# Kernel tuning notes

Hardware: AMD Instinct MI355X
Metric: run time of the kernel (lower is better)

Reference implementation:

```python
import jax, jax.numpy as jnp
import numpy as np

TEMPERATURE = 1.0
CLAMP = 10.0

def setup_inputs() -> dict:
    key = jax.random.key(0)
    k1, k2, kw, kb, km = jax.random.split(key, 5)
    B, N1, N2, D = 8, 2048, 2048, 256
    features1 = jax.random.normal(k1, (B, N1, D), dtype=jnp.float32)
    features2 = jax.random.normal(k2, (B, N2, D), dtype=jnp.float32)
    # Linear(D, D) params (torch convention: y = x @ W.T + b)
    W = jax.random.normal(kw, (D, D), dtype=jnp.float32) * (1.0 / np.sqrt(D))
    b = jax.random.normal(kb, (D,), dtype=jnp.float32) * 0.02
    # learnable metric matrix (initialized near identity, small perturbation)
    metric = jnp.eye(D, dtype=jnp.float32) + 0.01 * jax.random.normal(km, (D, D), dtype=jnp.float32)
    return {"features1": features1, "features2": features2, "W": W, "b": b, "metric": metric}

def reference(features1, features2, W, b, metric):
    # Linear transform (torch nn.Linear: x @ W.T + b)
    f1 = features1 @ W.T + b  # (B, N1, D)
    f2 = features2 @ W.T + b  # (B, N2, D)
    M = (metric + metric.T) * 0.5  # symmetrized metric (D, D)
    # Mahalanobis distance^2 expanded: d(x,y) = xMx + yMy - 2 xMy (valid since M symmetric)
    f1M = f1 @ M                                      # (B, N1, D)
    f2M = f2 @ M                                      # (B, N2, D)
    q1 = jnp.sum(f1M * f1, axis=-1)                   # (B, N1)
    q2 = jnp.sum(f2M * f2, axis=-1)                   # (B, N2)
    cross = jnp.einsum('bnd,bmd->bnm', f1M, f2)       # (B, N1, N2)
    dist_sq = q1[:, :, None] + q2[:, None, :] - 2.0 * cross
    stable = jnp.clip(-dist_sq / TEMPERATURE, -CLAMP, CLAMP)
    return jnp.exp(stable)
```

## Files before the change

### kernel.cpp

```cpp
#include <hip/hip_runtime.h>

#define DD 256
#define NBATCH 8
#define NROW 2048
#define TROWS (NBATCH*NROW)

typedef __attribute__((ext_vector_type(8))) short short8;
typedef __attribute__((ext_vector_type(4))) float f32x4;

__device__ __forceinline__ unsigned short f2bf(float f) {
  unsigned int u = __float_as_uint(f);
  u += 0x7FFFu + ((u >> 16) & 1u);
  return (unsigned short)(u >> 16);
}

__device__ __forceinline__ void gload_lds16(const unsigned short* g, unsigned short* l) {
  __builtin_amdgcn_global_load_lds(
      (const __attribute__((address_space(1))) unsigned int*)(const void*)g,
      (__attribute__((address_space(3))) unsigned int*)(void*)l,
      16, 0, 0);
}

__global__ void k_convert(const float* __restrict__ x1, const float* __restrict__ x2,
                          unsigned short* __restrict__ xb)
{
  const long long i = (long long)blockIdx.x * 256 + threadIdx.x;
  const long long base = i * 8;
  const long long n1 = (long long)TROWS * DD;
  const float* src = (base < n1) ? (x1 + base) : (x2 + (base - n1));
  float4 a = *(const float4*)(src);
  float4 b = *(const float4*)(src + 4);
  union { unsigned short us[8]; int4 v; } u;
  u.us[0]=f2bf(a.x); u.us[1]=f2bf(a.y); u.us[2]=f2bf(a.z); u.us[3]=f2bf(a.w);
  u.us[4]=f2bf(b.x); u.us[5]=f2bf(b.y); u.us[6]=f2bf(b.z); u.us[7]=f2bf(b.w);
  *(int4*)(xb + base) = u.v;
}

__global__ void k_prep(const float* __restrict__ metric, const float* __restrict__ W,
                       const float* __restrict__ bvec,
                       unsigned short* __restrict__ Wbf, unsigned short* __restrict__ WpT,
                       float* __restrict__ bp)
{
  __shared__ float msrow[DD];
  __shared__ float red[DD];
  const int e = blockIdx.x, d = threadIdx.x;
  msrow[d] = 0.5f * (metric[e*DD + d] + metric[d*DD + e]);
  Wbf[e*DD + d] = f2bf(W[e*DD + d]);
  __syncthreads();
  float acc = 0.f;
  for (int j = 0; j < DD; ++j) acc += msrow[j] * W[j*DD + d];
  WpT[e*DD + d] = f2bf(acc);
  red[d] = msrow[d] * bvec[d];
  __syncthreads();
  for (int s = 128; s; s >>= 1) { if (d < s) red[d] += red[d + s]; __syncthreads(); }
  if (d == 0) bp[e] = red[0];
}

__global__ __launch_bounds__(256, 2)
void k_fgemm(const unsigned short* __restrict__ x1b, const unsigned short* __restrict__ x2b,
             const unsigned short* __restrict__ B1, const unsigned short* __restrict__ B2,
             const float* __restrict__ bb, const float* __restrict__ bpv,
             unsigned short* __restrict__ o1, unsigned short* __restrict__ o2,
             float* __restrict__ qp1, float* __restrict__ qp2)
{
  __shared__ __align__(16) unsigned short As[2][128*32];
  __shared__ __align__(16) unsigned short B1s[2][128*32];
  __shared__ __align__(16) unsigned short B2s[2][128*32];
  __shared__ float bbs[128], bps[128];

  const int tid  = threadIdx.x;
  const int lane = tid & 63;
  const int wave = tid >> 6;
  const int wr = wave >> 1;
  const int wc = wave & 1;
  const int col0 = blockIdx.x * 128;
  const int row0 = blockIdx.y * 128;
  const int z    = blockIdx.z;

  const unsigned short* A = z ? x2b : x1b;
  unsigned short* outp    = z ? o2  : o1;
  float* qp               = z ? qp2 : qp1;

  if (tid < 128) bbs[tid]       = bb[col0 + tid];
  else           bps[tid - 128] = bpv[col0 + (tid - 128)];

  f32x4 accF[4][4], accM[4][4];
#pragma unroll
  for (int m = 0; m < 4; ++m)
#pragma unroll
    for (int n = 0; n < 4; ++n) { accF[m][n] = (f32x4){0,0,0,0}; accM[m][n] = (f32x4){0,0,0,0}; }

  const int lrow = lane >> 2;
  const int lkk  = (lane & 3) * 8;

#define STAGE_F(buf, k0) do { \
  _Pragma("unroll") \
  for (int c = 0; c < 2; ++c) { \
    const int chunk = wave * 2 + c; \
    const long long ra = (long long)(row0 + chunk*16 + lrow)*DD + (k0) + lkk; \
    const int rb = (col0 + chunk*16 + lrow)*DD + (k0) + lkk; \
    gload_lds16(A  + ra, &As[buf][chunk*512]); \
    gload_lds16(B1 + rb, &B1s[buf][chunk*512]); \
    gload_lds16(B2 + rb, &B2s[buf][chunk*512]); \
  } } while (0)

  STAGE_F(0, 0);
  __syncthreads();

  const int lr = lane & 15;
  const int lk = (lane >> 4) * 8;

#pragma unroll
  for (int kt = 0; kt < 8; ++kt) {
    const int cur = kt & 1;
    if (kt < 7) STAGE_F(cur ^ 1, (kt + 1) * 32);
    short8 af[4], b1f[4], b2f[4];
#pragma unroll
    for (int m = 0; m < 4; ++m) af[m]  = *(const short8*)&As[cur][(wr*64 + m*16 + lr)*32 + lk];
#pragma unroll
    for (int n = 0; n < 4; ++n) {
      b1f[n] = *(const short8*)&B1s[cur][(wc*64 + n*16 + lr)*32 + lk];
      b2f[n] = *(const short8*)&B2s[cur][(wc*64 + n*16 + lr)*32 + lk];
    }
#pragma unroll
    for (int m = 0; m < 4; ++m)
#pragma unroll
      for (int n = 0; n < 4; ++n) {
        accF[m][n] = __builtin_amdgcn_mfma_f32_16x16x32_bf16(af[m], b1f[n], accF[m][n], 0, 0, 0);
        accM[m][n] = __builtin_amdgcn_mfma_f32_16x16x32_bf16(af[m], b2f[n], accM[m][n], 0, 0, 0);
      }
    __syncthreads();
  }

#pragma unroll
  for (int m = 0; m < 4; ++m) {
#pragma unroll
    for (int r = 0; r < 4; ++r) {
      const int rowl = wr*64 + m*16 + (lane >> 4)*4 + r;
      float p = 0.f;
#pragma unroll
      for (int n = 0; n < 4; ++n) {
        const int coll = wc*64 + n*16 + (lane & 15);
        const float fv  = accF[m][n][r] + bbs[coll];
        const float fMv = accM[m][n][r] + bps[coll];
        p += fv * fMv;
        outp[(long long)(row0 + rowl)*DD + (col0 + coll)] = f2bf(z ? fv : fMv);
      }
      p += __shfl_xor(p, 1); p += __shfl_xor(p, 2);
      p += __shfl_xor(p, 4); p += __shfl_xor(p, 8);
      if ((lane & 15) == 0) qp[(blockIdx.x*2 + wc)*TROWS + row0 + rowl] = p;
    }
  }
#undef STAGE_F
}

__global__ __launch_bounds__(256, 2)
void k_cross(const unsigned short* __restrict__ f1M, const unsigned short* __restrict__ f2,
             const float* __restrict__ qp1, const float* __restrict__ qp2,
             float* __restrict__ out)
{
  __shared__ __align__(16) unsigned short As[2][128*32];
  __shared__ __align__(16) unsigned short Bs[2][128*32];
  __shared__ float q1s[128];
  __shared__ float q2s[128];

  const int tid  = threadIdx.x;
  const int lane = tid & 63;
  const int wave = tid >> 6;
  const int wr = wave >> 1;
  const int wc = wave & 1;

  const int bid = blockIdx.x;
  const int z  = bid & 7;
  const int t  = bid >> 3;
  const int bx = t & 15;
  const int by = t >> 4;
  const int row0 = by * 128;
  const int col0 = bx * 128;

  const unsigned short* A = f1M + (long long)z * NROW * DD;
  const unsigned short* B = f2  + (long long)z * NROW * DD;

  if (tid < 128) {
    const int rg = z*NROW + row0 + tid;
    q1s[tid] = qp1[rg] + qp1[TROWS + rg] + qp1[2*TROWS + rg] + qp1[3*TROWS + rg];
  } else {
    const int cg = z*NROW + col0 + (tid - 128);
    q2s[tid-128] = qp2[cg] + qp2[TROWS + cg] + qp2[2*TROWS + cg] + qp2[3*TROWS + cg];
  }

  f32x4 acc[4][4];
#pragma unroll
  for (int m = 0; m < 4; ++m)
#pragma unroll
    for (int n = 0; n < 4; ++n) acc[m][n] = (f32x4){0,0,0,0};

  const int lrow = lane >> 2;
  const int lkk  = (lane & 3) * 8;

#define STAGE_C(buf, k0) do { \
  _Pragma("unroll") \
  for (int c = 0; c < 2; ++c) { \
    const int chunk = wave * 2 + c; \
    gload_lds16(A + (long long)(row0 + chunk*16 + lrow)*DD + (k0) + lkk, &As[buf][chunk*512]); \
    gload_lds16(B + (long long)(col0 + chunk*16 + lrow)*DD + (k0) + lkk, &Bs[buf][chunk*512]); \
  } } while (0)

  STAGE_C(0, 0);
  __syncthreads();

  const int lr = lane & 15;
  const int lk = (lane >> 4) * 8;

#pragma unroll
  for (int kt = 0; kt < 8; ++kt) {
    const int cur = kt & 1;
    if (kt < 7) STAGE_C(cur ^ 1, (kt + 1) * 32);
    short8 af[4], bfr[4];
#pragma unroll
    for (int m = 0; m < 4; ++m) af[m]  = *(const short8*)&As[cur][(wr*64 + m*16 + lr)*32 + lk];
#pragma unroll
    for (int n = 0; n < 4; ++n) bfr[n] = *(const short8*)&Bs[cur][(wc*64 + n*16 + lr)*32 + lk];
#pragma unroll
    for (int m = 0; m < 4; ++m)
#pragma unroll
      for (int n = 0; n < 4; ++n)
        acc[m][n] = __builtin_amdgcn_mfma_f32_16x16x32_bf16(af[m], bfr[n], acc[m][n], 0, 0, 0);
    __syncthreads();
  }

  float* outz = out + (long long)z * NROW * NROW;
#pragma unroll
  for (int m = 0; m < 4; ++m) {
#pragma unroll
    for (int r = 0; r < 4; ++r) {
      const int rowl = wr*64 + m*16 + (lane >> 4)*4 + r;
#pragma unroll
      for (int n = 0; n < 4; ++n) {
        const int coll = wc*64 + n*16 + (lane & 15);
        const float dsq = q1s[rowl] + q2s[coll] - 2.0f * acc[m][n][r];
        const float sc = fminf(fmaxf(-dsq, -10.0f), 10.0f);
        outz[(long long)(row0 + rowl)*NROW + (col0 + coll)] = __expf(sc);
      }
    }
  }
#undef STAGE_C
}

extern "C" void kernel_launch(void* const* d_in, const int* in_sizes, int n_in,
                              void* d_out, int out_size, void* d_ws, size_t ws_size,
                              hipStream_t stream) {
  const float* x1     = (const float*)d_in[0];
  const float* x2     = (const float*)d_in[1];
  const float* W      = (const float*)d_in[2];
  const float* bv     = (const float*)d_in[3];
  const float* metric = (const float*)d_in[4];
  float* out = (float*)d_out;

  if (ws_size < 36000000) return;
  unsigned short* p   = (unsigned short*)d_ws;
  unsigned short* x1b = p; p += 4194304;
  unsigned short* x2b = p; p += 4194304;
  unsigned short* f1M = p; p += 4194304;
  unsigned short* f2  = p; p += 4194304;
  unsigned short* Wbf = p; p += 65536;
  unsigned short* WpT = p; p += 65536;
  float* fp  = (float*)p;
  float* qp1 = fp; fp += 4*TROWS;
  float* qp2 = fp; fp += 4*TROWS;
  float* bp  = fp; fp += 256;

  k_convert<<<4096, 256, 0, stream>>>(x1, x2, x1b);
  k_prep<<<256, 256, 0, stream>>>(metric, W, bv, Wbf, WpT, bp);
  dim3 gf(2, 128, 2);
  k_fgemm<<<gf, 256, 0, stream>>>(x1b, x2b, Wbf, WpT, bv, bp, f1M, f2, qp1, qp2);
  k_cross<<<2048, 256, 0, stream>>>(f1M, f2, qp1, qp2, out);
}
```

Before: 75.86 us.

## Fuse fp32-to-bf16 input conversion into feature GEMM with full-width column tiles

Removes the separate conversion kernel. The feature GEMM now loads fp32 inputs directly, converts them to bf16 in registers and writes them to LDS, with the global loads software-pipelined. Each block now covers 64 rows by all 256 columns, so each input row is read once instead of once per column tile. In exchange, LDS for the weight tiles grows and the grid shrinks to 512 blocks. The MFMA loops in both GEMMs are reordered to load B fragments one at a time, which lowers register pressure.

```diff
diff --git a/kernel.cpp b/kernel.cpp
--- a/kernel.cpp
+++ b/kernel.cpp
@@ -1,9 +1,8 @@
 #include <hip/hip_runtime.h>
 
 #define DD 256
-#define NBATCH 8
 #define NROW 2048
-#define TROWS (NBATCH*NROW)
+#define TROWS 16384
 
 typedef __attribute__((ext_vector_type(8))) short short8;
 typedef __attribute__((ext_vector_type(4))) float f32x4;
@@ -19,21 +18,6 @@
       (const __attribute__((address_space(1))) unsigned int*)(const void*)g,
       (__attribute__((address_space(3))) unsigned int*)(void*)l,
       16, 0, 0);
-}
-
-__global__ void k_convert(const float* __restrict__ x1, const float* __restrict__ x2,
-                          unsigned short* __restrict__ xb)
-{
-  const long long i = (long long)blockIdx.x * 256 + threadIdx.x;
-  const long long base = i * 8;
-  const long long n1 = (long long)TROWS * DD;
-  const float* src = (base < n1) ? (x1 + base) : (x2 + (base - n1));
-  float4 a = *(const float4*)(src);
-  float4 b = *(const float4*)(src + 4);
-  union { unsigned short us[8]; int4 v; } u;
-  u.us[0]=f2bf(a.x); u.us[1]=f2bf(a.y); u.us[2]=f2bf(a.z); u.us[3]=f2bf(a.w);
-  u.us[4]=f2bf(b.x); u.us[5]=f2bf(b.y); u.us[6]=f2bf(b.z); u.us[7]=f2bf(b.w);
-  *(int4*)(xb + base) = u.v;
 }
 
 __global__ void k_prep(const float* __restrict__ metric, const float* __restrict__ W,
@@ -57,32 +41,25 @@
 }
 
 __global__ __launch_bounds__(256, 2)
-void k_fgemm(const unsigned short* __restrict__ x1b, const unsigned short* __restrict__ x2b,
+void k_fgemm(const float* __restrict__ x1, const float* __restrict__ x2,
              const unsigned short* __restrict__ B1, const unsigned short* __restrict__ B2,
              const float* __restrict__ bb, const float* __restrict__ bpv,
              unsigned short* __restrict__ o1, unsigned short* __restrict__ o2,
              float* __restrict__ qp1, float* __restrict__ qp2)
 {
-  __shared__ __align__(16) unsigned short As[2][128*32];
-  __shared__ __align__(16) unsigned short B1s[2][128*32];
-  __shared__ __align__(16) unsigned short B2s[2][128*32];
-  __shared__ float bbs[128], bps[128];
+  __shared__ __align__(16) unsigned short As[2][64*32];
+  __shared__ __align__(16) unsigned short B1s[2][256*32];
+  __shared__ __align__(16) unsigned short B2s[2][256*32];
 
   const int tid  = threadIdx.x;
   const int lane = tid & 63;
   const int wave = tid >> 6;
-  const int wr = wave >> 1;
-  const int wc = wave & 1;
-  const int col0 = blockIdx.x * 128;
-  const int row0 = blockIdx.y * 128;
-  const int z    = blockIdx.z;
-
-  const unsigned short* A = z ? x2b : x1b;
-  unsigned short* outp    = z ? o2  : o1;
-  float* qp               = z ? qp2 : qp1;
-
-  if (tid < 128) bbs[tid]       = bb[col0 + tid];
-  else           bps[tid - 128] = bpv[col0 + (tid - 128)];
+  const int row0 = blockIdx.x * 64;
+  const int z    = blockIdx.y;
+
+  const float* X       = z ? x2 : x1;
+  unsigned short* outp = z ? o2 : o1;
+  float* qp            = z ? qp2 : qp1;
 
   f32x4 accF[4][4], accM[4][4];
 #pragma unroll
@@ -90,21 +67,35 @@
 #pragma unroll
     for (int n = 0; n < 4; ++n) { accF[m][n] = (f32x4){0,0,0,0}; accM[m][n] = (f32x4){0,0,0,0}; }
 
+  const int ar = tid >> 2;
+  const int ako = (tid & 3) * 8;
   const int lrow = lane >> 2;
   const int lkk  = (lane & 3) * 8;
 
-#define STAGE_F(buf, k0) do { \
+#define STAGE_B(buf, k0) do { \
   _Pragma("unroll") \
-  for (int c = 0; c < 2; ++c) { \
-    const int chunk = wave * 2 + c; \
-    const long long ra = (long long)(row0 + chunk*16 + lrow)*DD + (k0) + lkk; \
-    const int rb = (col0 + chunk*16 + lrow)*DD + (k0) + lkk; \
-    gload_lds16(A  + ra, &As[buf][chunk*512]); \
+  for (int c = 0; c < 4; ++c) { \
+    const int chunk = wave * 4 + c; \
+    const int rb = (chunk*16 + lrow)*DD + (k0) + lkk; \
     gload_lds16(B1 + rb, &B1s[buf][chunk*512]); \
     gload_lds16(B2 + rb, &B2s[buf][chunk*512]); \
   } } while (0)
 
-  STAGE_F(0, 0);
+#define LOAD_A(k0) \
+  float4 a0 = *(const float4*)(X + (long long)(row0 + ar)*DD + (k0) + ako); \
+  float4 a1 = *(const float4*)(X + (long long)(row0 + ar)*DD + (k0) + ako + 4)
+
+#define CVT_WRITE_A(buf) do { \
+  union { unsigned short us[8]; int4 v; } u; \
+  u.us[0]=f2bf(a0.x); u.us[1]=f2bf(a0.y); u.us[2]=f2bf(a0.z); u.us[3]=f2bf(a0.w); \
+  u.us[4]=f2bf(a1.x); u.us[5]=f2bf(a1.y); u.us[6]=f2bf(a1.z); u.us[7]=f2bf(a1.w); \
+  *(int4*)&As[buf][ar*32 + ako] = u.v; } while (0)
+
+  {
+    LOAD_A(0);
+    STAGE_B(0, 0);
+    CVT_WRITE_A(0);
+  }
   __syncthreads();
 
   const int lr = lane & 15;
@@ -113,45 +104,71 @@
 #pragma unroll
   for (int kt = 0; kt < 8; ++kt) {
     const int cur = kt & 1;
-    if (kt < 7) STAGE_F(cur ^ 1, (kt + 1) * 32);
-    short8 af[4], b1f[4], b2f[4];
-#pragma unroll
-    for (int m = 0; m < 4; ++m) af[m]  = *(const short8*)&As[cur][(wr*64 + m*16 + lr)*32 + lk];
-#pragma unroll
-    for (int n = 0; n < 4; ++n) {
-      b1f[n] = *(const short8*)&B1s[cur][(wc*64 + n*16 + lr)*32 + lk];
-      b2f[n] = *(const short8*)&B2s[cur][(wc*64 + n*16 + lr)*32 + lk];
-    }
-#pragma unroll
-    for (int m = 0; m < 4; ++m)
-#pragma unroll
-      for (int n = 0; n < 4; ++n) {
-        accF[m][n] = __builtin_amdgcn_mfma_f32_16x16x32_bf16(af[m], b1f[n], accF[m][n], 0, 0, 0);
-        accM[m][n] = __builtin_amdgcn_mfma_f32_16x16x32_bf16(af[m], b2f[n], accM[m][n], 0, 0, 0);
-      }
+    if (kt < 7) {
+      const int k0 = (kt + 1) * 32;
+      LOAD_A(k0);
+      STAGE_B(cur ^ 1, k0);
+      short8 af[4];
+#pragma unroll
+      for (int m = 0; m < 4; ++m) af[m] = *(const short8*)&As[cur][(m*16 + lr)*32 + lk];
+#pragma unroll
+      for (int n = 0; n < 4; ++n) {
+        const short8 b1 = *(const short8*)&B1s[cur][(wave*64 + n*16 + lr)*32 + lk];
+        const short8 b2 = *(const short8*)&B2s[cur][(wave*64 + n*16 + lr)*32 + lk];
+#pragma unroll
+        for (int m = 0; m < 4; ++m) {
+          accF[m][n] = __builtin_amdgcn_mfma_f32_16x16x32_bf16(af[m], b1, accF[m][n], 0, 0, 0);
+          accM[m][n] = __builtin_amdgcn_mfma_f32_16x16x32_bf16(af[m], b2, accM[m][n], 0, 0, 0);
+        }
+      }
+      CVT_WRITE_A(cur ^ 1);
+    } else {
+      short8 af[4];
+#pragma unroll
+      for (int m = 0; m < 4; ++m) af[m] = *(const short8*)&As[cur][(m*16 + lr)*32 + lk];
+#pragma unroll
+      for (int n = 0; n < 4; ++n) {
+        const short8 b1 = *(const short8*)&B1s[cur][(wave*64 + n*16 + lr)*32 + lk];
+        const short8 b2 = *(const short8*)&B2s[cur][(wave*64 + n*16 + lr)*32 + lk];
+#pragma unroll
+        for (int m = 0; m < 4; ++m) {
+          accF[m][n] = __builtin_amdgcn_mfma_f32_16x16x32_bf16(af[m], b1, accF[m][n], 0, 0, 0);
+          accM[m][n] = __builtin_amdgcn_mfma_f32_16x16x32_bf16(af[m], b2, accM[m][n], 0, 0, 0);
+        }
+      }
+    }
     __syncthreads();
   }
 
+  float bbv[4], bpv4[4];
+#pragma unroll
+  for (int n = 0; n < 4; ++n) {
+    const int coll = wave*64 + n*16 + (lane & 15);
+    bbv[n]  = bb[coll];
+    bpv4[n] = bpv[coll];
+  }
 #pragma unroll
   for (int m = 0; m < 4; ++m) {
 #pragma unroll
     for (int r = 0; r < 4; ++r) {
-      const int rowl = wr*64 + m*16 + (lane >> 4)*4 + r;
+      const int rowl = m*16 + (lane >> 4)*4 + r;
       float p = 0.f;
 #pragma unroll
       for (int n = 0; n < 4; ++n) {
-        const int coll = wc*64 + n*16 + (lane & 15);
-        const float fv  = accF[m][n][r] + bbs[coll];
-        const float fMv = accM[m][n][r] + bps[coll];
+        const int coll = wave*64 + n*16 + (lane & 15);
+        const float fv  = accF[m][n][r] + bbv[n];
+        const float fMv = accM[m][n][r] + bpv4[n];
         p += fv * fMv;
-        outp[(long long)(row0 + rowl)*DD + (col0 + coll)] = f2bf(z ? fv : fMv);
+        outp[(long long)(row0 + rowl)*DD + coll] = f2bf(z ? fv : fMv);
       }
       p += __shfl_xor(p, 1); p += __shfl_xor(p, 2);
       p += __shfl_xor(p, 4); p += __shfl_xor(p, 8);
-      if ((lane & 15) == 0) qp[(blockIdx.x*2 + wc)*TROWS + row0 + rowl] = p;
-    }
-  }
-#undef STAGE_F
+      if ((lane & 15) == 0) qp[wave*TROWS + row0 + rowl] = p;
+    }
+  }
+#undef STAGE_B
+#undef LOAD_A
+#undef CVT_WRITE_A
 }
 
 __global__ __launch_bounds__(256, 2)
@@ -216,16 +233,16 @@
   for (int kt = 0; kt < 8; ++kt) {
     const int cur = kt & 1;
     if (kt < 7) STAGE_C(cur ^ 1, (kt + 1) * 32);
-    short8 af[4], bfr[4];
-#pragma unroll
-    for (int m = 0; m < 4; ++m) af[m]  = *(const short8*)&As[cur][(wr*64 + m*16 + lr)*32 + lk];
-#pragma unroll
-    for (int n = 0; n < 4; ++n) bfr[n] = *(const short8*)&Bs[cur][(wc*64 + n*16 + lr)*32 + lk];
-#pragma unroll
-    for (int m = 0; m < 4; ++m)
-#pragma unroll
-      for (int n = 0; n < 4; ++n)
-        acc[m][n] = __builtin_amdgcn_mfma_f32_16x16x32_bf16(af[m], bfr[n], acc[m][n], 0, 0, 0);
+    short8 af[4];
+#pragma unroll
+    for (int m = 0; m < 4; ++m) af[m] = *(const short8*)&As[cur][(wr*64 + m*16 + lr)*32 + lk];
+#pragma unroll
+    for (int n = 0; n < 4; ++n) {
+      const short8 bfr = *(const short8*)&Bs[cur][(wc*64 + n*16 + lr)*32 + lk];
+#pragma unroll
+      for (int m = 0; m < 4; ++m)
+        acc[m][n] = __builtin_amdgcn_mfma_f32_16x16x32_bf16(af[m], bfr, acc[m][n], 0, 0, 0);
+    }
     __syncthreads();
   }
 
@@ -257,22 +274,19 @@
   const float* metric = (const float*)d_in[4];
   float* out = (float*)d_out;
 
-  if (ws_size < 36000000) return;
+  if (ws_size < 20000000) return;
   unsigned short* p   = (unsigned short*)d_ws;
-  unsigned short* x1b = p; p += 4194304;
-  unsigned short* x2b = p; p += 4194304;
-  unsigned short* f1M = p; p += 4194304;
-  unsigned short* f2  = p; p += 4194304;
-  unsigned short* Wbf = p; p += 65536;
-  unsigned short* WpT = p; p += 65536;
+  unsigned short* f1M = p; p += (size_t)TROWS*DD;
+  unsigned short* f2  = p; p += (size_t)TROWS*DD;
+  unsigned short* Wbf = p; p += DD*DD;
+  unsigned short* WpT = p; p += DD*DD;
   float* fp  = (float*)p;
   float* qp1 = fp; fp += 4*TROWS;
   float* qp2 = fp; fp += 4*TROWS;
   float* bp  = fp; fp += 256;
 
-  k_convert<<<4096, 256, 0, stream>>>(x1, x2, x1b);
   k_prep<<<256, 256, 0, stream>>>(metric, W, bv, Wbf, WpT, bp);
-  dim3 gf(2, 128, 2);
-  k_fgemm<<<gf, 256, 0, stream>>>(x1b, x2b, Wbf, WpT, bv, bp, f1M, f2, qp1, qp2);
+  dim3 gf(256, 2);
+  k_fgemm<<<gf, 256, 0, stream>>>(x1, x2, Wbf, WpT, bv, bp, f1M, f2, qp1, qp2);
   k_cross<<<2048, 256, 0, stream>>>(f1M, f2, qp1, qp2, out);
 }
```

Result: faster. 71.07 us (-6.3%).
